# Performance work log

Hardware: AMD Instinct MI355X
Metric: run time of the kernel (lower is better)

The kernel has to match this reference:

```python
import jax, jax.numpy as jnp
import numpy as np

N_NODE = 40000  # item vocabulary
H = 100         # hidden size (SR-GNN default)
B = 64          # sessions per batch
L = 16          # items per session (equal-length sessions)
N = B * L       # total graph nodes
E = 2048        # total edges
NL = 1          # GatedGraphConv layers


def setup_inputs() -> dict:
    key = jax.random.key(0)
    ks = jax.random.split(key, 20)
    stdv = 1.0 / np.sqrt(H)
    u = lambda k, shape: jax.random.uniform(k, shape, jnp.float32, -stdv, stdv)
    return {
        "x": jax.random.randint(ks[0], (N,), 0, N_NODE),
        "edge_index": jax.random.randint(ks[1], (2, E), 0, N),
        "edge_weight": jax.random.uniform(ks[2], (E,), jnp.float32),
        "batch": jnp.arange(N) // L,  # node -> session id, equal-length sessions
        "embed": u(ks[3], (N_NODE, H)),
        "ggc_w": u(ks[4], (NL, H, H)),
        "gru_wih": u(ks[5], (3 * H, H)),
        "gru_whh": u(ks[6], (3 * H, H)),
        "gru_bih": u(ks[7], (3 * H,)),
        "gru_bhh": u(ks[8], (3 * H,)),
        "W1_w": u(ks[9], (H, H)), "W1_b": u(ks[10], (H,)),
        "W2_w": u(ks[11], (H, H)), "W2_b": u(ks[12], (H,)),
        "Wt_w": u(ks[13], (H, H)), "Wt_b": u(ks[14], (H,)),
        "q_w": u(ks[15], (1, H)), "q_b": u(ks[16], (1,)),
        "W3_w": u(ks[17], (H, 2 * H)), "W3_b": u(ks[18], (H,)),
    }


def reference(x, edge_index, edge_weight, batch, embed, ggc_w, gru_wih, gru_whh,
              gru_bih, gru_bhh, W1_w, W1_b, W2_w, W2_b, Wt_w, Wt_b, q_w, q_b,
              W3_w, W3_b):
    # Embedding lookup
    h = embed[x]  # [N, H]
    src, dst = edge_index[0], edge_index[1]
    # GatedGraphConv: weighted message aggregation + GRUCell update
    for l in range(NL):
        m = h @ ggc_w[l]                                             # [N, H]
        agg = jnp.zeros_like(h).at[dst].add(edge_weight[:, None] * m[src])
        gi = agg @ gru_wih.T + gru_bih                               # [N, 3H]
        gh = h @ gru_whh.T + gru_bhh
        ir, iz, inn = jnp.split(gi, 3, axis=-1)
        hr, hz, hn = jnp.split(gh, 3, axis=-1)
        r = jax.nn.sigmoid(ir + hr)
        zg = jax.nn.sigmoid(iz + hz)
        ng = jnp.tanh(inn + r * hn)
        h = (1.0 - zg) * ng + zg * h
    v = h.reshape(B, L, H)                                           # sessions
    s_l = v[:, -1]                                                   # [B, H] last item
    # alpha = q(sigmoid(W1(v_n) + W2(v)))
    a = jax.nn.sigmoid((s_l @ W1_w.T + W1_b)[:, None, :] + (v @ W2_w.T + W2_b))
    alpha = a @ q_w.T + q_b                                          # [B, L, 1]
    s_g = jnp.sum(alpha * v, axis=1)                                 # [B, H]
    s_h = jnp.concatenate([s_l, s_g], axis=-1) @ W3_w.T + W3_b       # [B, H]
    # Target attention: s_t[b] = softmax(E @ W_t(v_b)^T, -1) @ v_b, contracted
    # directly against E to avoid materializing [B, N_NODE, H].
    vt = v @ Wt_w.T + Wt_b                                           # [B, L, H]
    P = jax.nn.softmax(jnp.einsum('jh,blh->bjl', embed, vt), axis=-1)
    C = jnp.einsum('blh,jh->bjl', v, embed)                          # v_l . E_j
    z = s_h @ embed.T + jnp.sum(P * C, axis=-1)                      # [B, N_NODE]
    return z
```

## Files before the change

### kernel.cpp

```cpp
#include <hip/hip_runtime.h>
#include <hip/hip_bf16.h>

#define Hh    100
#define NN    1024
#define BB    64
#define LL    16
#define EE    2048
#define NNODE 40000

#define BSPL  8
#define BPB   (BB / BSPL)
#define PFR   8
#define PPAN  (PFR * 64 * 8)
#define GJ    4
#define EBS   104
#define GRB   2

typedef unsigned short u16;
typedef __attribute__((ext_vector_type(8))) short short8;
typedef __attribute__((ext_vector_type(4))) float f32x4;

__device__ __forceinline__ float bf2f(u16 u) {
    union { unsigned int i; float f; } v;
    v.i = ((unsigned int)u) << 16;
    return v.f;
}

__device__ __forceinline__ u16 f2bf(float f) {
    unsigned int x = __float_as_uint(f);
    unsigned int lsb = (x >> 16) & 1u;
    x += 0x7fffu + lsb;
    return (u16)(x >> 16);
}

__device__ __forceinline__ float sigmoidf_(float x) {
    return 1.0f / (1.0f + expf(-x));
}

template <bool BF>
__device__ __forceinline__ float ldv(const void* p, size_t i) {
    if (BF) return bf2f(((const u16*)p)[i]);
    return ((const float*)p)[i];
}
__device__ __forceinline__ float ldvf(int flag, const void* p, size_t i) {
    return flag ? ldv<true>(p, i) : ldv<false>(p, i);
}

template <bool BF>
__device__ void cvt_impl(int t,
                         const void* ew, const void* ggc, const void* wih, const void* whh,
                         const void* bih, const void* bhh, const void* W1w, const void* W1b,
                         const void* W2w, const void* W2b, const void* Wtw, const void* Wtb,
                         const void* qw, const void* qb, const void* W3w, const void* W3b,
                         float* __restrict__ W) {
    const void* src; int si; int doff; int di;
    if      (t <   2048) { src = ew;  si = t;          doff = 0;      di = si; }
    else if (t <  12048) { src = ggc; si = t - 2048;   doff = 2048;   di = si; }
    else if (t <  42048) { src = wih; si = t - 12048;  doff = 12048;  { int r = si / 100, k = si - r * 100; di = k * 800 + (r % 100) * 8 + r / 100; } }
    else if (t <  72048) { src = whh; si = t - 42048;  doff = 12048;  { int r = si / 100, k = si - r * 100; di = k * 800 + (r % 100) * 8 + 3 + r / 100; } }
    else if (t <  72348) { src = bih; si = t - 72048;  doff = 92048;  di = si; }
    else if (t <  72648) { src = bhh; si = t - 72348;  doff = 92352;  di = si; }
    else if (t <  82648) { src = W1w; si = t - 72648;  doff = 92656;  di = (si % 100) * 100 + si / 100; }
    else if (t <  82748) { src = W1b; si = t - 82648;  doff = 102656; di = si; }
    else if (t <  92748) { src = W2w; si = t - 82748;  doff = 102768; di = (si % 100) * 100 + si / 100; }
    else if (t <  92848) { src = W2b; si = t - 92748;  doff = 112768; di = si; }
    else if (t < 102848) { src = Wtw; si = t - 92848;  doff = 112880; di = (si % 100) * 100 + si / 100; }
    else if (t < 102948) { src = Wtb; si = t - 102848; doff = 122880; di = si; }
    else if (t < 103048) { src = qw;  si = t - 102948; doff = 122992; di = si; }
    else if (t < 103049) { src = qb;  si = t - 103048; doff = 123104; di = si; }
    else if (t < 123049) { src = W3w; si = t - 103049; doff = 123120; di = (si % 200) * 100 + si / 200; }
    else                 { src = W3b; si = t - 123049; doff = 143120; di = si; }
    W[doff + di] = ldv<BF>(src, si);
}

__global__ void __launch_bounds__(256) k_cvt(const void* embed_raw, int* __restrict__ flag,
                      const void* ew, const void* ggc, const void* wih, const void* whh,
                      const void* bih, const void* bhh, const void* W1w, const void* W1b,
                      const void* W2w, const void* W2b, const void* Wtw, const void* Wtb,
                      const void* qw, const void* qb, const void* W3w, const void* W3b,
                      float* __restrict__ W, float* __restrict__ agg0,
                      u16* __restrict__ SD, u16* __restrict__ EB) {
    __shared__ int cnt;
    if (threadIdx.x == 0) cnt = 0;
    __syncthreads();
    const u16* eb16 = (const u16*)embed_raw;
    {
        float v = bf2f(eb16[threadIdx.x]);
        if (!(fabsf(v) <= 0.5f)) atomicAdd(&cnt, 1);
    }
    __syncthreads();
    const bool bf = (cnt == 0);
    const int bid = blockIdx.x;
    if (bid == 0 && threadIdx.x == 0) flag[0] = bf ? 1 : 0;
    if (bid < 482) {
        int t = bid * 256 + threadIdx.x;
        if (t < NN * Hh) agg0[t] = 0.0f;
        if (t < 8192) ((unsigned int*)SD)[t] = 0u;
        if (t >= 123149) return;
        if (bf) cvt_impl<true >(t, ew, ggc, wih, whh, bih, bhh, W1w, W1b, W2w, W2b, Wtw, Wtb, qw, qb, W3w, W3b, W);
        else    cvt_impl<false>(t, ew, ggc, wih, whh, bih, bhh, W1w, W1b, W2w, W2b, Wtw, Wtb, qw, qb, W3w, W3b, W);
    } else {
        int t = (bid - 482) * 256 + threadIdx.x;
        const int total = (NNODE + 1) * (EBS / 2);
        if (t >= total) return;
        int r = t / (EBS / 2), c2 = t - r * (EBS / 2);
        int k0 = c2 * 2;
        unsigned int w = 0;
        if (r < NNODE && k0 + 1 < Hh) {
            if (bf) {
                w = *(const unsigned int*)&((const u16*)embed_raw)[(size_t)r * Hh + k0];
            } else {
                float2 e2 = *(const float2*)&((const float*)embed_raw)[(size_t)r * Hh + k0];
                w = (unsigned int)f2bf(e2.x) | ((unsigned int)f2bf(e2.y) << 16);
            }
        }
        ((unsigned int*)EB)[t] = w;
    }
}

__global__ void k_scatter2(const int* __restrict__ flag, const int* __restrict__ ei,
                           const float* __restrict__ ew, const int* __restrict__ x,
                           const void* __restrict__ embed, float* __restrict__ agg0) {
    int t = blockIdx.x * 256 + threadIdx.x;
    if (t >= EE * (Hh / 2)) return;
    int e = t / (Hh / 2), j2 = t - e * (Hh / 2);
    int j = j2 * 2;
    int src = ei[e], dst = ei[EE + e];
    const int fl = flag[0];
    float w = ew[e];
    float h0, h1v;
    size_t base = (size_t)x[src] * Hh + j;
    if (fl) {
        unsigned int u = *(const unsigned int*)&((const u16*)embed)[base];
        h0 = bf2f((u16)(u & 0xffff));
        h1v = bf2f((u16)(u >> 16));
    } else {
        float2 f2 = *(const float2*)&((const float*)embed)[base];
        h0 = f2.x; h1v = f2.y;
    }
    atomicAdd(&agg0[dst * Hh + j], w * h0);
    atomicAdd(&agg0[dst * Hh + j + 1], w * h1v);
}

__global__ void __launch_bounds__(512) k_gruatt(const int* __restrict__ flag,
                      const int* __restrict__ x, const void* __restrict__ embed,
                      const float* __restrict__ agg0, const float* __restrict__ ggc_f,
                      const float* __restrict__ wC,
                      const float* __restrict__ bih, const float* __restrict__ bhh,
                      const float* __restrict__ W1T, const float* __restrict__ W1b,
                      const float* __restrict__ W2T, const float* __restrict__ W2b,
                      const float* __restrict__ WtT, const float* __restrict__ Wtb,
                      float* __restrict__ h1, float* __restrict__ Q2g,
                      float* __restrict__ Q1g, u16* __restrict__ P) {
    __shared__ float sG[GRB * Hh];
    __shared__ float sH0[GRB * Hh];
    __shared__ float sA[GRB * Hh];
    __shared__ float sV[GRB * Hh];
    __shared__ float sVT[GRB * Hh];
    __shared__ float sPx[6 * 512];
    const int tid = threadIdx.x;
    const int r0 = blockIdx.x * GRB;
    const int fl = flag[0];
    const int kh = tid >> 8;
    const int o  = tid & 255;
    const bool valid = (o < GRB * Hh);
    const int i = o / Hh, j = o - i * Hh;
    const int k0 = kh * 50, k1 = k0 + 50;

    if (tid < GRB * Hh) {
        sG[tid] = agg0[r0 * Hh + tid];
    } else if (tid < 2 * GRB * Hh) {
        int o2 = tid - GRB * Hh;
        int i2 = o2 / Hh, j2 = o2 - i2 * Hh;
        sH0[o2] = ldvf(fl, embed, (size_t)x[r0 + i2] * Hh + j2);
    }
    __syncthreads();

    {
        float acc = 0.0f;
        if (valid) {
            const float* gi = sG + i * Hh;
#pragma unroll 5
            for (int k = k0; k < k1; ++k) acc += gi[k] * ggc_f[k * Hh + j];
        }
        sPx[tid] = acc;
    }
    __syncthreads();
    if (valid && kh == 0) sA[o] = sPx[tid] + sPx[tid + 256];
    __syncthreads();

    {
        float p0 = 0, p1 = 0, p2 = 0, p3 = 0, p4 = 0, p5 = 0;
        if (valid) {
            const float* ai = sA + i * Hh;
            const float* hi = sH0 + i * Hh;
            const float* wbase = wC + j * 8;
#pragma unroll 5
            for (int k = k0; k < k1; ++k) {
                float a = ai[k], h = hi[k];
                const float* wr = wbase + k * 800;
                float4 w0 = *(const float4*)wr;
                float2 w1 = *(const float2*)(wr + 4);
                p0 += a * w0.x;
                p1 += a * w0.y;
                p2 += a * w0.z;
                p3 += h * w0.w;
                p4 += h * w1.x;
                p5 += h * w1.y;
            }
        }
        sPx[tid] = p0;             sPx[512 + tid] = p1;
        sPx[1024 + tid] = p2;      sPx[1536 + tid] = p3;
        sPx[2048 + tid] = p4;      sPx[2560 + tid] = p5;
    }
    __syncthreads();
    if (valid && kh == 0) {
        float s_ir = bih[j] + sPx[tid] + sPx[tid + 256];
        float s_iz = bih[j + Hh] + sPx[512 + tid] + sPx[512 + tid + 256];
        float s_in = bih[j + 2 * Hh] + sPx[1024 + tid] + sPx[1024 + tid + 256];
        float s_hr = bhh[j] + sPx[1536 + tid] + sPx[1536 + tid + 256];
        float s_hz = bhh[j + Hh] + sPx[2048 + tid] + sPx[2048 + tid + 256];
        float s_hn = bhh[j + 2 * Hh] + sPx[2560 + tid] + sPx[2560 + tid + 256];
        float r = sigmoidf_(s_ir + s_hr);
        float z = sigmoidf_(s_iz + s_hz);
        float n = tanhf(s_in + r * s_hn);
        float hv = (1.0f - z) * n + z * sH0[o];
        sV[o] = hv;
        h1[r0 * Hh + o] = hv;
    }
    __syncthreads();

    {
        float a2 = 0.0f, at = 0.0f;
        if (valid) {
            const float* vi = sV + i * Hh;
#pragma unroll 5
            for (int k = k0; k < k1; ++k) {
                float vk = vi[k];
                a2 += vk * W2T[k * Hh + j];
                at += vk * WtT[k * Hh + j];
            }
        }
        sPx[tid] = a2;
        sPx[512 + tid] = at;
    }
    __syncthreads();
    if (valid && kh == 0) {
        Q2g[r0 * Hh + o] = sPx[tid] + sPx[tid + 256] + W2b[j];
        sVT[o] = sPx[512 + tid] + sPx[512 + tid + 256] + Wtb[j];
    }
    __syncthreads();

    if ((r0 & 15) == 14 && tid < Hh) {
        const float* vl = sV + Hh;
        float a1 = 0.0f;
#pragma unroll 4
        for (int k = 0; k < Hh; ++k) a1 += vl[k] * W1T[k * Hh + tid];
        Q1g[(r0 >> 4) * Hh + tid] = a1 + W1b[tid];
    }
    const int b = r0 >> 4;
    if (tid < GRB * 2 * 4 * 4) {
        int ii = tid >> 5, rest = tid & 31;
        int tt = rest >> 4, ks = (rest >> 2) & 3, qq = rest & 3;
        int mm = (r0 & 15) + ii;
        int col0 = ks * 32 + qq * 8;
        const float* srow = (tt == 0 ? sVT : sV) + ii * Hh;
        short8 t8;
#pragma unroll
        for (int e = 0; e < 8; ++e) {
            int col = col0 + e;
            t8[e] = (short)f2bf(col < Hh ? srow[col] : 0.0f);
        }
        *(short8*)&P[((size_t)b * PFR + tt * 4 + ks) * 512 + (qq * 16 + mm) * 8] = t8;
    }
}

__global__ void __launch_bounds__(256) k_att2(const float* __restrict__ h1,
                    const float* __restrict__ Q1g, const float* __restrict__ Q2g,
                    const float* __restrict__ qw, const float* __restrict__ qb,
                    const float* __restrict__ W3T, const float* __restrict__ W3b,
                    u16* __restrict__ SD) {
    __shared__ float V[LL * Hh];
    __shared__ float AL[LL];
    __shared__ float SG[Hh];
    __shared__ float SH[Hh];
    const int b = blockIdx.x, tid = threadIdx.x;
    for (int o = tid; o < LL * Hh; o += 256) V[o] = h1[b * LL * Hh + o];
    __syncthreads();
    {
        int l = tid >> 4, t = tid & 15;
        float acc = 0.0f;
        for (int j = t; j < Hh; j += 16)
            acc += sigmoidf_(Q1g[b * Hh + j] + Q2g[(b * LL + l) * Hh + j]) * qw[j];
        acc += __shfl_xor(acc, 8);
        acc += __shfl_xor(acc, 4);
        acc += __shfl_xor(acc, 2);
        acc += __shfl_xor(acc, 1);
        if (t == 0) AL[l] = acc + qb[0];
    }
    __syncthreads();
    if (tid < Hh) {
        float acc = 0.0f;
#pragma unroll
        for (int l = 0; l < LL; ++l) acc += AL[l] * V[l * Hh + tid];
        SG[tid] = acc;
    }
    __syncthreads();
    if (tid < Hh) {
        float acc = W3b[tid];
#pragma unroll 4
        for (int k = 0; k < Hh; ++k) acc += V[(LL - 1) * Hh + k] * W3T[k * Hh + tid];
#pragma unroll 4
        for (int k = 0; k < Hh; ++k) acc += SG[k] * W3T[(Hh + k) * Hh + tid];
        SH[tid] = acc;
    }
    __syncthreads();
    if (tid < 128) {
        int ks = tid >> 5, qq = (tid >> 3) & 3, e = tid & 7;
        int col = ks * 32 + qq * 8 + e;
        float v = (col < Hh) ? SH[col] : 0.0f;
        SD[(((size_t)(b >> 3) * 4 + ks) * 64 + qq * 16 + (b & 7)) * 8 + e] = f2bf(v);
    }
}

__device__ __forceinline__ short8 load_efrag(const void* embed, bool bf, int j, int k0) {
    short8 v = {0, 0, 0, 0, 0, 0, 0, 0};
    if (j >= NNODE || k0 >= Hh) return v;
    if (bf) {
        const u16* row = (const u16*)embed + (size_t)j * Hh + k0;
        if (k0 + 8 <= Hh) {
            ushort4 a = *(const ushort4*)(row);
            ushort4 b = *(const ushort4*)(row + 4);
            v[0] = (short)a.x; v[1] = (short)a.y; v[2] = (short)a.z; v[3] = (short)a.w;
            v[4] = (short)b.x; v[5] = (short)b.y; v[6] = (short)b.z; v[7] = (short)b.w;
        } else {
            for (int e = 0; e < Hh - k0; ++e) v[e] = (short)row[e];
        }
    } else {
        const float* row = (const float*)embed + (size_t)j * Hh + k0;
        if (k0 + 8 <= Hh) {
            float4 a = *(const float4*)(row);
            float4 b = *(const float4*)(row + 4);
            v[0] = (short)f2bf(a.x); v[1] = (short)f2bf(a.y); v[2] = (short)f2bf(a.z); v[3] = (short)f2bf(a.w);
            v[4] = (short)f2bf(b.x); v[5] = (short)f2bf(b.y); v[6] = (short)f2bf(b.z); v[7] = (short)f2bf(b.w);
        } else {
            for (int e = 0; e < Hh - k0; ++e) v[e] = (short)f2bf(row[e]);
        }
    }
    return v;
}

#define JBLK  157

template <int EMODE>
__global__ void __launch_bounds__(256) k_score(const int* __restrict__ flag,
                                               const void* __restrict__ embed,
                                               const u16* __restrict__ EB,
                                               const u16* __restrict__ P,
                                               const u16* __restrict__ SD,
                                               void* __restrict__ out) {
    __shared__ alignas(16) u16 sPan[2][PPAN];
    const int jb = blockIdx.x * 256;
    const int slice = blockIdx.y;
    const int b0 = slice * BPB;
    const int tid = threadIdx.x;
    const bool bf = (flag[0] != 0);
    const int wave = tid >> 6, lane = tid & 63;
    const int m = lane & 15, quad = lane >> 4;

    short8 Bf[GJ][4];
#pragma unroll
    for (int g = 0; g < GJ; ++g)
#pragma unroll
        for (int ks = 0; ks < 4; ++ks) {
            int j = jb + wave * 64 + g * 16 + m;
            if (EMODE) {
                short8 v = {0, 0, 0, 0, 0, 0, 0, 0};
                if (j < NNODE)
                    v = *(const short8*)&EB[(size_t)j * EBS + ks * 32 + quad * 8];
                Bf[g][ks] = v;
            } else {
                Bf[g][ks] = load_efrag(embed, bf, j, ks * 32 + quad * 8);
            }
        }

    short8 Sf[4];
#pragma unroll
    for (int ks = 0; ks < 4; ++ks)
        Sf[ks] = *(const short8*)&SD[(((size_t)slice * 4 + ks) * 64 + lane) * 8];
    f32x4 accsd[GJ];
#pragma unroll
    for (int g = 0; g < GJ; ++g) {
        accsd[g] = (f32x4){0.0f, 0.0f, 0.0f, 0.0f};
#pragma unroll
        for (int ks = 0; ks < 4; ++ks)
            accsd[g] = __builtin_amdgcn_mfma_f32_16x16x32_bf16(Sf[ks], Bf[g][ks], accsd[g], 0, 0, 0);
    }

    {
        const uint4* s4 = (const uint4*)(P + (size_t)b0 * PPAN);
        uint4 g0 = s4[tid], g1 = s4[tid + 256];
        uint4* d = (uint4*)sPan[0];
        d[tid] = g0; d[tid + 256] = g1;
    }
    __syncthreads();

    int cur = 0;
    for (int bi = 0; bi < BPB; ++bi) {
        const int b = b0 + bi;
        uint4 g0, g1;
        if (bi + 1 < BPB) {
            const uint4* s4 = (const uint4*)(P + (size_t)(b + 1) * PPAN);
            g0 = s4[tid]; g1 = s4[tid + 256];
        }

        const u16* sp = sPan[cur];
        f32x4 acc[GJ][2];
#pragma unroll
        for (int g = 0; g < GJ; ++g)
#pragma unroll
            for (int t = 0; t < 2; ++t)
                acc[g][t] = (f32x4){0.0f, 0.0f, 0.0f, 0.0f};
#pragma unroll
        for (int t = 0; t < 2; ++t) {
            short8 A0 = *(const short8*)&sp[(t * 4 + 0) * 512 + lane * 8];
            short8 A1 = *(const short8*)&sp[(t * 4 + 1) * 512 + lane * 8];
            short8 A2 = *(const short8*)&sp[(t * 4 + 2) * 512 + lane * 8];
            short8 A3 = *(const short8*)&sp[(t * 4 + 3) * 512 + lane * 8];
#pragma unroll
            for (int g = 0; g < GJ; ++g) {
                acc[g][t] = __builtin_amdgcn_mfma_f32_16x16x32_bf16(A0, Bf[g][0], acc[g][t], 0, 0, 0);
                acc[g][t] = __builtin_amdgcn_mfma_f32_16x16x32_bf16(A1, Bf[g][1], acc[g][t], 0, 0, 0);
                acc[g][t] = __builtin_amdgcn_mfma_f32_16x16x32_bf16(A2, Bf[g][2], acc[g][t], 0, 0, 0);
                acc[g][t] = __builtin_amdgcn_mfma_f32_16x16x32_bf16(A3, Bf[g][3], acc[g][t], 0, 0, 0);
            }
        }

#pragma unroll
        for (int g = 0; g < GJ; ++g) {
            float den = 0.0f, num = 0.0f;
#pragma unroll
            for (int r = 0; r < 4; ++r) {
                float p = __expf(acc[g][0][r]);
                den += p;
                num += p * acc[g][1][r];
            }
            den += __shfl_xor(den, 16); num += __shfl_xor(num, 16);
            den += __shfl_xor(den, 32); num += __shfl_xor(num, 32);
            f32x4 s4v = accsd[g];
            int rr = bi & 3;
            float sdv = (rr == 0) ? s4v[0] : (rr == 1) ? s4v[1] : (rr == 2) ? s4v[2] : s4v[3];
            sdv = __shfl(sdv, ((bi >> 2) << 4) | m);
            if (quad == 0) {
                int j = jb + wave * 64 + g * 16 + m;
                if (j < NNODE) {
                    float z = sdv + num / den;
                    if (bf) ((u16*)out)[(size_t)b * NNODE + j] = f2bf(z);
                    else    ((float*)out)[(size_t)b * NNODE + j] = z;
                }
            }
        }

        if (bi + 1 < BPB) {
            uint4* d = (uint4*)sPan[cur ^ 1];
            d[tid] = g0; d[tid + 256] = g1;
        }
        __syncthreads();
        cur ^= 1;
    }
}

extern "C" void kernel_launch(void* const* d_in, const int* in_sizes, int n_in,
                              void* d_out, int out_size, void* d_ws, size_t ws_size,
                              hipStream_t stream) {
    const int* x      = (const int*)d_in[0];
    const int* ei     = (const int*)d_in[1];
    const void* ew    = d_in[2];
    const void* embed = d_in[4];
    const void* ggc   = d_in[5];
    const void* wih   = d_in[6];
    const void* whh   = d_in[7];
    const void* bih   = d_in[8];
    const void* bhh   = d_in[9];
    const void* W1w   = d_in[10];
    const void* W1b   = d_in[11];
    const void* W2w   = d_in[12];
    const void* W2b   = d_in[13];
    const void* Wtw   = d_in[14];
    const void* Wtb   = d_in[15];
    const void* qw    = d_in[16];
    const void* qb    = d_in[17];
    const void* W3w   = d_in[18];
    const void* W3b   = d_in[19];
    float* ws = (float*)d_ws;
    int* flag = (int*)d_ws;

    float* W = ws + 64;
    float* ew_f  = W + 0;
    float* ggc_f = W + 2048;
    float* wC    = W + 12048;
    float* bih_f = W + 92048;
    float* bhh_f = W + 92352;
    float* W1T   = W + 92656;
    float* W1b_f = W + 102656;
    float* W2T   = W + 102768;
    float* W2b_f = W + 112768;
    float* WtT   = W + 112880;
    float* Wtb_f = W + 122880;
    float* qw_f  = W + 122992;
    float* qb_f  = W + 123104;
    float* W3T   = W + 123120;
    float* W3b_f = W + 143120;

    float* D     = ws + 143296;
    float* agg0  = D;
    float* h1    = D + 102400;
    float* Q2g   = D + 204800;
    float* Q1g   = D + 307200;
    u16*   P     = (u16*)(D + 313600);
    u16*   SDp   = (u16*)(D + 444672);
    u16*   EB    = (u16*)(D + 452864);

    const size_t need_bytes = (size_t)(143296 + 452864) * 4 + (size_t)(NNODE + 1) * EBS * 2;
    const bool emode = (ws_size >= need_bytes);

    const int ecvt_blocks = ((NNODE + 1) * (EBS / 2) + 255) / 256;
    k_cvt    <<<dim3(emode ? 482 + ecvt_blocks : 482), dim3(256), 0, stream>>>(
                                                   embed, flag, ew, ggc, wih, whh, bih, bhh,
                                                   W1w, W1b, W2w, W2b, Wtw, Wtb, qw, qb, W3w, W3b,
                                                   W, agg0, SDp, EB);
    k_scatter2<<<dim3(EE * (Hh / 2) / 256, 1), dim3(256), 0, stream>>>(flag, ei, ew_f, x, embed, agg0);
    k_gruatt <<<dim3(NN / GRB), dim3(512), 0, stream>>>(flag, x, embed, agg0, ggc_f, wC, bih_f, bhh_f,
                                                        W1T, W1b_f, W2T, W2b_f, WtT, Wtb_f,
                                                        h1, Q2g, Q1g, P);
    k_att2   <<<dim3(BB), dim3(256), 0, stream>>>(h1, Q1g, Q2g, qw_f, qb_f, W3T, W3b_f, SDp);
    if (emode)
        k_score<1><<<dim3(JBLK, BSPL), dim3(256), 0, stream>>>(flag, embed, EB, P, SDp, d_out);
    else
        k_score<0><<<dim3(JBLK, BSPL), dim3(256), 0, stream>>>(flag, embed, EB, P, SDp, d_out);
}
```

Before: 192.6 us.

## Fuse session attention into score kernel and skip EB repack for bf16

Removes the separate k_att2 launch and recomputes alpha, s_g and s_h for each block's 8 sessions inside k_score before building the MFMA A-fragments. It also skips the embedding repack into EB when inputs are already bf16 and reads embed directly in that case. This saves one launch plus the SD round trip, but every score block (JBLK×8 blocks) now redundantly recomputes the 8×100×200 W3 matvec and the attention weights before its main loop, which adds latency to each block.

```diff
diff --git a/kernel.cpp b/kernel.cpp
--- a/kernel.cpp
+++ b/kernel.cpp
@@ -79,7 +79,7 @@
                       const void* W2w, const void* W2b, const void* Wtw, const void* Wtb,
                       const void* qw, const void* qb, const void* W3w, const void* W3b,
                       float* __restrict__ W, float* __restrict__ agg0,
-                      u16* __restrict__ SD, u16* __restrict__ EB) {
+                      u16* __restrict__ EB) {
     __shared__ int cnt;
     if (threadIdx.x == 0) cnt = 0;
     __syncthreads();
@@ -95,11 +95,11 @@
     if (bid < 482) {
         int t = bid * 256 + threadIdx.x;
         if (t < NN * Hh) agg0[t] = 0.0f;
-        if (t < 8192) ((unsigned int*)SD)[t] = 0u;
         if (t >= 123149) return;
         if (bf) cvt_impl<true >(t, ew, ggc, wih, whh, bih, bhh, W1w, W1b, W2w, W2b, Wtw, Wtb, qw, qb, W3w, W3b, W);
         else    cvt_impl<false>(t, ew, ggc, wih, whh, bih, bhh, W1w, W1b, W2w, W2b, Wtw, Wtb, qw, qb, W3w, W3b, W);
     } else {
+        if (bf) return;
         int t = (bid - 482) * 256 + threadIdx.x;
         const int total = (NNODE + 1) * (EBS / 2);
         if (t >= total) return;
@@ -107,12 +107,8 @@
         int k0 = c2 * 2;
         unsigned int w = 0;
         if (r < NNODE && k0 + 1 < Hh) {
-            if (bf) {
-                w = *(const unsigned int*)&((const u16*)embed_raw)[(size_t)r * Hh + k0];
-            } else {
-                float2 e2 = *(const float2*)&((const float*)embed_raw)[(size_t)r * Hh + k0];
-                w = (unsigned int)f2bf(e2.x) | ((unsigned int)f2bf(e2.y) << 16);
-            }
+            float2 e2 = *(const float2*)&((const float*)embed_raw)[(size_t)r * Hh + k0];
+            w = (unsigned int)f2bf(e2.x) | ((unsigned int)f2bf(e2.y) << 16);
         }
         ((unsigned int*)EB)[t] = w;
     }
@@ -275,54 +271,6 @@
     }
 }
 
-__global__ void __launch_bounds__(256) k_att2(const float* __restrict__ h1,
-                    const float* __restrict__ Q1g, const float* __restrict__ Q2g,
-                    const float* __restrict__ qw, const float* __restrict__ qb,
-                    const float* __restrict__ W3T, const float* __restrict__ W3b,
-                    u16* __restrict__ SD) {
-    __shared__ float V[LL * Hh];
-    __shared__ float AL[LL];
-    __shared__ float SG[Hh];
-    __shared__ float SH[Hh];
-    const int b = blockIdx.x, tid = threadIdx.x;
-    for (int o = tid; o < LL * Hh; o += 256) V[o] = h1[b * LL * Hh + o];
-    __syncthreads();
-    {
-        int l = tid >> 4, t = tid & 15;
-        float acc = 0.0f;
-        for (int j = t; j < Hh; j += 16)
-            acc += sigmoidf_(Q1g[b * Hh + j] + Q2g[(b * LL + l) * Hh + j]) * qw[j];
-        acc += __shfl_xor(acc, 8);
-        acc += __shfl_xor(acc, 4);
-        acc += __shfl_xor(acc, 2);
-        acc += __shfl_xor(acc, 1);
-        if (t == 0) AL[l] = acc + qb[0];
-    }
-    __syncthreads();
-    if (tid < Hh) {
-        float acc = 0.0f;
-#pragma unroll
-        for (int l = 0; l < LL; ++l) acc += AL[l] * V[l * Hh + tid];
-        SG[tid] = acc;
-    }
-    __syncthreads();
-    if (tid < Hh) {
-        float acc = W3b[tid];
-#pragma unroll 4
-        for (int k = 0; k < Hh; ++k) acc += V[(LL - 1) * Hh + k] * W3T[k * Hh + tid];
-#pragma unroll 4
-        for (int k = 0; k < Hh; ++k) acc += SG[k] * W3T[(Hh + k) * Hh + tid];
-        SH[tid] = acc;
-    }
-    __syncthreads();
-    if (tid < 128) {
-        int ks = tid >> 5, qq = (tid >> 3) & 3, e = tid & 7;
-        int col = ks * 32 + qq * 8 + e;
-        float v = (col < Hh) ? SH[col] : 0.0f;
-        SD[(((size_t)(b >> 3) * 4 + ks) * 64 + qq * 16 + (b & 7)) * 8 + e] = f2bf(v);
-    }
-}
-
 __device__ __forceinline__ short8 load_efrag(const void* embed, bool bf, int j, int k0) {
     short8 v = {0, 0, 0, 0, 0, 0, 0, 0};
     if (j >= NNODE || k0 >= Hh) return v;
@@ -357,9 +305,18 @@
                                                const void* __restrict__ embed,
                                                const u16* __restrict__ EB,
                                                const u16* __restrict__ P,
-                                               const u16* __restrict__ SD,
+                                               const float* __restrict__ h1,
+                                               const float* __restrict__ Q1g,
+                                               const float* __restrict__ Q2g,
+                                               const float* __restrict__ qw,
+                                               const float* __restrict__ qb,
+                                               const float* __restrict__ W3T,
+                                               const float* __restrict__ W3b,
                                                void* __restrict__ out) {
     __shared__ alignas(16) u16 sPan[2][PPAN];
+    __shared__ float sAL[BPB][LL];
+    __shared__ float sSG[BPB * Hh];
+    __shared__ float sSH[BPB * Hh];
     const int jb = blockIdx.x * 256;
     const int slice = blockIdx.y;
     const int b0 = slice * BPB;
@@ -374,20 +331,66 @@
 #pragma unroll
         for (int ks = 0; ks < 4; ++ks) {
             int j = jb + wave * 64 + g * 16 + m;
-            if (EMODE) {
+            if (bf) {
+                Bf[g][ks] = load_efrag(embed, true, j, ks * 32 + quad * 8);
+            } else if (EMODE) {
                 short8 v = {0, 0, 0, 0, 0, 0, 0, 0};
                 if (j < NNODE)
                     v = *(const short8*)&EB[(size_t)j * EBS + ks * 32 + quad * 8];
                 Bf[g][ks] = v;
             } else {
-                Bf[g][ks] = load_efrag(embed, bf, j, ks * 32 + quad * 8);
-            }
-        }
+                Bf[g][ks] = load_efrag(embed, false, j, ks * 32 + quad * 8);
+            }
+        }
+
+    {
+        int p = tid >> 1, hf = tid & 1;
+        int bb = p >> 4, l = p & 15;
+        const float* q1 = Q1g + (size_t)(b0 + bb) * Hh;
+        const float* q2 = Q2g + ((size_t)(b0 + bb) * LL + l) * Hh;
+        float acc = 0.0f;
+        int js = hf * 50;
+        for (int j = js; j < js + 50; ++j)
+            acc += sigmoidf_(q1[j] + q2[j]) * qw[j];
+        acc += __shfl_xor(acc, 1);
+        if (hf == 0) sAL[bb][l] = acc + qb[0];
+    }
+    __syncthreads();
+    for (int it = tid; it < BPB * Hh; it += 256) {
+        int bb = it / Hh, k = it - bb * Hh;
+        const float* vb = h1 + ((size_t)(b0 + bb) * LL) * Hh + k;
+        float acc = 0.0f;
+#pragma unroll
+        for (int l = 0; l < LL; ++l) acc += sAL[bb][l] * vb[l * Hh];
+        sSG[it] = acc;
+    }
+    __syncthreads();
+    for (int it = tid; it < BPB * Hh; it += 256) {
+        int bb = it / Hh, c = it - bb * Hh;
+        const float* vl = h1 + ((size_t)(b0 + bb) * LL + (LL - 1)) * Hh;
+        const float* sg = sSG + bb * Hh;
+        float acc = W3b[c];
+#pragma unroll 4
+        for (int k = 0; k < Hh; ++k) acc += vl[k] * W3T[k * Hh + c];
+#pragma unroll 4
+        for (int k = 0; k < Hh; ++k) acc += sg[k] * W3T[(Hh + k) * Hh + c];
+        sSH[it] = acc;
+    }
+    __syncthreads();
 
     short8 Sf[4];
 #pragma unroll
-    for (int ks = 0; ks < 4; ++ks)
-        Sf[ks] = *(const short8*)&SD[(((size_t)slice * 4 + ks) * 64 + lane) * 8];
+    for (int ks = 0; ks < 4; ++ks) {
+        short8 t8 = {0, 0, 0, 0, 0, 0, 0, 0};
+        if (m < BPB) {
+#pragma unroll
+            for (int e = 0; e < 8; ++e) {
+                int col = ks * 32 + quad * 8 + e;
+                t8[e] = (short)f2bf(col < Hh ? sSH[m * Hh + col] : 0.0f);
+            }
+        }
+        Sf[ks] = t8;
+    }
     f32x4 accsd[GJ];
 #pragma unroll
     for (int g = 0; g < GJ; ++g) {
@@ -518,24 +521,24 @@
     float* Q2g   = D + 204800;
     float* Q1g   = D + 307200;
     u16*   P     = (u16*)(D + 313600);
-    u16*   SDp   = (u16*)(D + 444672);
-    u16*   EB    = (u16*)(D + 452864);
-
-    const size_t need_bytes = (size_t)(143296 + 452864) * 4 + (size_t)(NNODE + 1) * EBS * 2;
+    u16*   EB    = (u16*)(D + 444672);
+
+    const size_t need_bytes = (size_t)(143296 + 444672) * 4 + (size_t)(NNODE + 1) * EBS * 2;
     const bool emode = (ws_size >= need_bytes);
 
     const int ecvt_blocks = ((NNODE + 1) * (EBS / 2) + 255) / 256;
     k_cvt    <<<dim3(emode ? 482 + ecvt_blocks : 482), dim3(256), 0, stream>>>(
                                                    embed, flag, ew, ggc, wih, whh, bih, bhh,
                                                    W1w, W1b, W2w, W2b, Wtw, Wtb, qw, qb, W3w, W3b,
-                                                   W, agg0, SDp, EB);
+                                                   W, agg0, EB);
     k_scatter2<<<dim3(EE * (Hh / 2) / 256, 1), dim3(256), 0, stream>>>(flag, ei, ew_f, x, embed, agg0);
     k_gruatt <<<dim3(NN / GRB), dim3(512), 0, stream>>>(flag, x, embed, agg0, ggc_f, wC, bih_f, bhh_f,
                                                         W1T, W1b_f, W2T, W2b_f, WtT, Wtb_f,
                                                         h1, Q2g, Q1g, P);
-    k_att2   <<<dim3(BB), dim3(256), 0, stream>>>(h1, Q1g, Q2g, qw_f, qb_f, W3T, W3b_f, SDp);
     if (emode)
-        k_score<1><<<dim3(JBLK, BSPL), dim3(256), 0, stream>>>(flag, embed, EB, P, SDp, d_out);
+        k_score<1><<<dim3(JBLK, BSPL), dim3(256), 0, stream>>>(flag, embed, EB, P, h1, Q1g, Q2g,
+                                                               qw_f, qb_f, W3T, W3b_f, d_out);
     else
-        k_score<0><<<dim3(JBLK, BSPL), dim3(256), 0, stream>>>(flag, embed, EB, P, SDp, d_out);
-}
+        k_score<0><<<dim3(JBLK, BSPL), dim3(256), 0, stream>>>(flag, embed, EB, P, h1, Q1g, Q2g,
+                                                               qw_f, qb_f, W3T, W3b_f, d_out);
+}
```

After: 267.5 us. 38.9% more time.
